# Performance work log

Hardware: AMD Instinct MI355X
Metric: run time of the kernel (lower is better)

The kernel has to match this reference:

```python
import jax, jax.numpy as jnp
import numpy as np

EPS = 1e-8
LAM = 1.0


def setup_inputs() -> dict:
    key = jax.random.key(0)
    k1, k2 = jax.random.split(key)
    B, H, W = 32, 512, 512
    output = jax.random.normal(k1, (B, 1, H, W), dtype=jnp.float32)
    target = jax.random.normal(k2, (B, 1, H, W), dtype=jnp.float32)
    return {"output": output, "target": target}


def _frc_loss(output, target):
    # squeeze channel dim: (B,1,H,W) -> (B,H,W)
    output = output[:, 0]
    target = target[:, 0]
    B, H, W = output.shape
    rnyquist = H // 2

    # radial index map (H,W): round(sqrt(fx^2 + fy^2)) in pixel-frequency units
    fx = jnp.fft.fftfreq(H, 1.0 / H)
    fy = jnp.fft.fftfreq(W, 1.0 / W)
    X, Y = jnp.meshgrid(fx, fy, indexing='ij')
    radial = jnp.round(jnp.sqrt(X ** 2 + Y ** 2)).astype(jnp.int32)
    # bins > rnyquist were ignored by the original loop -> dump into extra bin
    idx = jnp.where(radial > rnyquist, rnyquist + 1, radial).reshape(-1)  # (H*W,)

    F1 = jnp.fft.fft2(output, norm='forward')  # (B,H,W) complex
    F2 = jnp.fft.fft2(target, norm='forward')

    # per-pixel correlation terms, laid out (HW, B) for segment_sum over leading axis
    a = (F1.real * F2.real + F1.imag * F2.imag).reshape(B, -1).T
    b = (F1.imag * F2.real - F1.real * F2.imag).reshape(B, -1).T
    c1 = (F1.real ** 2 + F1.imag ** 2).reshape(B, -1).T
    c2 = (F2.real ** 2 + F2.imag ** 2).reshape(B, -1).T
    stacked = jnp.stack([a, b, c1, c2], axis=-1)  # (HW, B, 4)

    # single-pass radial-bin segment sum (replaces O(R*H*W) masked loop)
    sums = jax.ops.segment_sum(stacked, idx, num_segments=rnyquist + 2)
    sums = sums[:rnyquist + 1]  # drop overflow bin -> (rnyquist+1, B, 4)
    C_r, C_i, C1, C2 = sums[..., 0], sums[..., 1], sums[..., 2], sums[..., 3]

    frc = jnp.sqrt(C_r ** 2 + C_i ** 2) / (jnp.sqrt(C1 * C2) + EPS)
    return LAM * jnp.mean((1.0 - frc) ** 2)


def reference(output, target):
    return _frc_loss(output, target)
```

## Files before the change

kernel.cpp:

```cpp
#include <hip/hip_runtime.h>
#include <math.h>

#define NIMG 32
#define NB3  771
#define NSLICE (NIMG * 8)
#define PI_F 3.14159265358979323846f

__device__ __forceinline__ float2 cadd(float2 a, float2 b){ return make_float2(a.x+b.x, a.y+b.y); }
__device__ __forceinline__ float2 csub(float2 a, float2 b){ return make_float2(a.x-b.x, a.y-b.y); }
__device__ __forceinline__ float2 cmul(float2 a, float2 b){ return make_float2(a.x*b.x - a.y*b.y, a.x*b.y + a.y*b.x); }
__device__ __forceinline__ float2 cmul_mi(float2 a){ return make_float2(a.y, -a.x); }
__device__ __forceinline__ float2 tw(const float2* T, int m){ return T[m + (m >> 3)]; }
__device__ __forceinline__ int   sw(int pos){ return pos + (pos >> 3); }

__device__ __forceinline__ void dft8(float2* x) {
    const float c = 0.70710678118654752f;
    float2 u0 = cadd(x[0], x[4]), u1 = cadd(x[1], x[5]);
    float2 u2 = cadd(x[2], x[6]), u3 = cadd(x[3], x[7]);
    float2 v0 = csub(x[0], x[4]);
    float2 d1 = csub(x[1], x[5]);
    float2 v1 = make_float2(c*(d1.x + d1.y), c*(d1.y - d1.x));
    float2 d2 = csub(x[2], x[6]);
    float2 v2 = make_float2(d2.y, -d2.x);
    float2 d3 = csub(x[3], x[7]);
    float2 v3 = make_float2(-c*(d3.x - d3.y), -c*(d3.x + d3.y));
    float2 e0 = cadd(u0,u2), e1 = cadd(u1,u3);
    float2 f0 = csub(u0,u2), f1 = cmul_mi(csub(u1,u3));
    float2 g0 = cadd(v0,v2), g1 = cadd(v1,v3);
    float2 h0 = csub(v0,v2), h1 = cmul_mi(csub(v1,v3));
    x[0] = cadd(e0,e1); x[4] = csub(e0,e1);
    x[2] = cadd(f0,f1); x[6] = csub(f0,f1);
    x[1] = cadd(g0,g1); x[5] = csub(g0,g1);
    x[3] = cadd(h0,h1); x[7] = csub(h0,h1);
}

__device__ __forceinline__ void wave_fft512_dual(float2* Xa, float2* Xb,
                                                 float2* Sw, const float2* T,
                                                 int J) {
    dft8(Xa);
    dft8(Xb);
#pragma unroll
    for (int k = 1; k < 8; ++k) Xa[k] = cmul(Xa[k], tw(T, J * k));
#pragma unroll
    for (int k = 1; k < 8; ++k) Xb[k] = cmul(Xb[k], tw(T, J * k));
    const int jj = J + (J >> 3);
    const int j2 = J & 7;
    const int bb = 72 * (J >> 3) + j2;

#pragma unroll
    for (int k = 0; k < 8; ++k) Sw[jj + 72*k] = Xa[k];
#pragma unroll
    for (int q = 0; q < 8; ++q) Xa[q] = Sw[bb + 9*q];
#pragma unroll
    for (int k = 0; k < 8; ++k) Sw[jj + 72*k] = Xb[k];
#pragma unroll
    for (int q = 0; q < 8; ++q) Xb[q] = Sw[bb + 9*q];

    dft8(Xa);
    dft8(Xb);
#pragma unroll
    for (int k = 1; k < 8; ++k) Xa[k] = cmul(Xa[k], tw(T, 8 * j2 * k));
#pragma unroll
    for (int k = 1; k < 8; ++k) Xb[k] = cmul(Xb[k], tw(T, 8 * j2 * k));

#pragma unroll
    for (int k = 0; k < 8; ++k) Sw[bb + 9*k] = Xa[k];
#pragma unroll
    for (int q = 0; q < 8; ++q) Xa[q] = Sw[9*J + q];
#pragma unroll
    for (int k = 0; k < 8; ++k) Sw[bb + 9*k] = Xb[k];
#pragma unroll
    for (int q = 0; q < 8; ++q) Xb[q] = Sw[9*J + q];

    dft8(Xa);
    dft8(Xb);
}

__global__ __launch_bounds__(512) void fft_rows_T(const float* __restrict__ xr,
                                                  const float* __restrict__ yr,
                                                  float2* __restrict__ Zt,
                                                  float* __restrict__ sums,
                                                  unsigned int* __restrict__ counter) {
    __shared__ float2 S[8 * 576];
    __shared__ float2 T[576];
    const int t = threadIdx.x, w = t >> 6, J = t & 63;
    const int im = blockIdx.x >> 5, grp = blockIdx.x & 31;

    if (blockIdx.x < NSLICE) {
        float* z = sums + (size_t)blockIdx.x * NB3;
        for (int i = t; i < NB3; i += 512) z[i] = 0.0f;
        if (blockIdx.x == 0 && t == 0) *counter = 0u;
    }

    {
        float s, c;
        __sincosf(-2.0f * PI_F * (float)t / 512.0f, &s, &c);
        T[t + (t >> 3)] = make_float2(c, s);
    }

    const size_t b0 = ((size_t)(im * 512 + grp * 16 + w)) << 9;
    const size_t b1 = b0 + ((size_t)8 << 9);
    float2 X0[8], X1[8];
#pragma unroll
    for (int q = 0; q < 8; ++q) {
        X0[q] = make_float2(xr[b0 + J + 64*q], yr[b0 + J + 64*q]);
        X1[q] = make_float2(xr[b1 + J + 64*q], yr[b1 + J + 64*q]);
    }
    __syncthreads();

    float2* Sw = S + w * 576;
    wave_fft512_dual(X0, X1, Sw, T, J);

    const int r = ((J & 7) << 3) | (J >> 3);

#pragma unroll
    for (int k = 0; k < 8; ++k) Sw[64*k + r] = X0[k];
    __syncthreads();
    float2 eA[8];
#pragma unroll
    for (int j = 0; j < 8; ++j) eA[j] = S[j*576 + t];
    __syncthreads();

#pragma unroll
    for (int k = 0; k < 8; ++k) Sw[64*k + r] = X1[k];
    __syncthreads();
    float2 eB[8];
#pragma unroll
    for (int j = 0; j < 8; ++j) eB[j] = S[j*576 + t];

    float4* o = (float4*)(Zt + ((size_t)im << 18) + ((size_t)t << 9)
                             + (size_t)(grp * 16));
    o[0] = make_float4(eA[0].x, eA[0].y, eA[1].x, eA[1].y);
    o[1] = make_float4(eA[2].x, eA[2].y, eA[3].x, eA[3].y);
    o[2] = make_float4(eA[4].x, eA[4].y, eA[5].x, eA[5].y);
    o[3] = make_float4(eA[6].x, eA[6].y, eA[7].x, eA[7].y);
    o[4] = make_float4(eB[0].x, eB[0].y, eB[1].x, eB[1].y);
    o[5] = make_float4(eB[2].x, eB[2].y, eB[3].x, eB[3].y);
    o[6] = make_float4(eB[4].x, eB[4].y, eB[5].x, eB[5].y);
    o[7] = make_float4(eB[6].x, eB[6].y, eB[7].x, eB[7].y);
}

__global__ __launch_bounds__(256) void fft_cols_rings(const float2* __restrict__ Zt,
                                                      float* __restrict__ sums,
                                                      unsigned int* __restrict__ counter,
                                                      float* __restrict__ out) {
    __shared__ float2 S[4 * 576];
    __shared__ float2 T[576];
    __shared__ float  bins[258 * 3];
    __shared__ int    lastFlag;
    const int t = threadIdx.x, w = t >> 6, J = t & 63;
    const int im = blockIdx.x >> 6, g = blockIdx.x & 63;
    const int p = 4 * g + w;

#pragma unroll
    for (int i = 0; i < 2; ++i) {
        const int m = t + 256 * i;
        float s, c;
        __sincosf(-2.0f * PI_F * (float)m / 512.0f, &s, &c);
        T[m + (m >> 3)] = make_float2(c, s);
    }
    for (int i = t; i < 258 * 3; i += 256) bins[i] = 0.0f;

    const int c0 = (p == 0) ? 0   : p;
    const int c1 = (p == 0) ? 256 : 512 - p;
    const float2* rp0 = Zt + ((size_t)im << 18) + ((size_t)c0 << 9);
    const float2* rp1 = Zt + ((size_t)im << 18) + ((size_t)c1 << 9);
    float2 X0[8], X1[8];
#pragma unroll
    for (int q = 0; q < 8; ++q) { X0[q] = rp0[J + 64*q]; X1[q] = rp1[J + 64*q]; }
    __syncthreads();

    float2* A = S + w * 576;
    const int r  = ((J & 7) << 3) | (J >> 3);
    const int pk = r + (r >> 3);

    const float scale = 1.0f / (512.0f * 512.0f);
    auto pix = [&](float2 zk, float2 zm, float& av, float& c1v, float& c2v) {
        float f1r = 0.5f * (zk.x + zm.x) * scale;
        float f1i = 0.5f * (zk.y - zm.y) * scale;
        float f2r = 0.5f * (zk.y + zm.y) * scale;
        float f2i = 0.5f * (zm.x - zk.x) * scale;
        av  = f1r * f2r + f1i * f2i;
        c1v = f1r * f1r + f1i * f1i;
        c2v = f2r * f2r + f2i * f2i;
    };
    auto flush = [&](int ring, float a, float b, float c) {
        if (ring >= 0 && ring <= 256) {
            unsafeAtomicAdd(&bins[ring*3+0], a);
            unsafeAtomicAdd(&bins[ring*3+1], b);
            unsafeAtomicAdd(&bins[ring*3+2], c);
        }
    };

    wave_fft512_dual(X0, X1, A, T, J);

#pragma unroll
    for (int k = 0; k < 8; ++k) A[72*k + pk] = X0[k];

    float2 asv[8];
    if (p == 0) {
        int cur0 = -1;
        float a0 = 0, b0 = 0, c0v = 0;
#pragma unroll
        for (int i = 0; i < 8; ++i) {
            const int ky  = 8*J + i;
            const int kyp = (512 - ky) & 511;
            float2 zk = A[sw(ky)], zm = A[sw(kyp)];
            const float fk = (ky < 256) ? (float)ky : (float)(ky - 512);
            float av, cv, dv;
            pix(zk, zm, av, cv, dv);
            int rr = (int)rintf(fabsf(fk)); if (rr > 256) rr = 257;
            if (rr != cur0) { flush(cur0, a0, b0, c0v); cur0 = rr; a0 = av; b0 = cv; c0v = dv; }
            else            { a0 += av; b0 += cv; c0v += dv; }
        }
        flush(cur0, a0, b0, c0v);
    } else {
#pragma unroll
        for (int i = 0; i < 8; ++i) asv[i] = A[9*J + i];
    }

#pragma unroll
    for (int k = 0; k < 8; ++k) A[72*k + pk] = X1[k];

    if (p == 0) {
        int cur1 = -1;
        float a1 = 0, b1 = 0, c1v = 0;
#pragma unroll
        for (int i = 0; i < 8; ++i) {
            const int ky  = 8*J + i;
            const int kyp = (512 - ky) & 511;
            float2 zk = A[sw(ky)], zm = A[sw(kyp)];
            const float fk = (ky < 256) ? (float)ky : (float)(ky - 512);
            float av, cv, dv;
            pix(zk, zm, av, cv, dv);
            int rr = (int)rintf(sqrtf(fk*fk + 65536.0f)); if (rr > 256) rr = 257;
            if (rr != cur1) { flush(cur1, a1, b1, c1v); cur1 = rr; a1 = av; b1 = cv; c1v = dv; }
            else            { a1 += av; b1 += cv; c1v += dv; }
        }
        flush(cur1, a1, b1, c1v);
    } else {
        const float fy2 = (float)p * (float)p;
        int curR = -1;
        float sA = 0, sB = 0, sC = 0;
#pragma unroll
        for (int i = 0; i < 8; ++i) {
            const int ky  = 8*J + i;
            const int kyp = (512 - ky) & 511;
            float2 zk = asv[i];
            float2 zm = A[sw(kyp)];
            float a1v, b1v, d1v;
            pix(zk, zm, a1v, b1v, d1v);
            const float fk = (ky < 256) ? (float)ky : (float)(ky - 512);
            int rr = (int)rintf(sqrtf(fk*fk + fy2)); if (rr > 256) rr = 257;
            const float aa = 2.0f*a1v, bb = 2.0f*b1v, cc = 2.0f*d1v;
            if (rr != curR) { flush(curR, sA, sB, sC); curR = rr; sA = aa; sB = bb; sC = cc; }
            else            { sA += aa; sB += bb; sC += cc; }
        }
        flush(curR, sA, sB, sC);
    }
    __syncthreads();

    {
        float* dst = sums + (size_t)(im * 8 + (g & 7)) * NB3;
        for (int i = t; i < NB3; i += 256) unsafeAtomicAdd(&dst[i], bins[i]);
    }

    __syncthreads();
    if (t == 0) {
        __threadfence();
        unsigned int old = atomicAdd(counter, 1u);
        lastFlag = (old == (unsigned int)(gridDim.x - 1)) ? 1 : 0;
    }
    __syncthreads();
    if (lastFlag) {
        __threadfence();
        float acc = 0.0f;
        for (int idx = t; idx < NIMG * 257; idx += 256) {
            const int imQ = idx / 257;
            const int rr  = idx - imQ * 257;
            const float* pp = sums + (size_t)imQ * 8 * NB3 + rr * 3;
            float cr = 0.f, c1s = 0.f, c2s = 0.f;
#pragma unroll
            for (int s = 0; s < 8; ++s) {
                cr  += pp[(size_t)s * NB3 + 0];
                c1s += pp[(size_t)s * NB3 + 1];
                c2s += pp[(size_t)s * NB3 + 2];
            }
            float frc = fabsf(cr) / (sqrtf(c1s * c2s) + 1e-8f);
            float d = 1.0f - frc;
            acc += d * d;
        }
#pragma unroll
        for (int off = 32; off > 0; off >>= 1) acc += __shfl_down(acc, off);
        __shared__ float red[4];
        if ((t & 63) == 0) red[t >> 6] = acc;
        __syncthreads();
        if (t == 0)
            out[0] = (red[0] + red[1] + red[2] + red[3]) *
                     (1.0f / (257.0f * (float)NIMG));
    }
}

extern "C" void kernel_launch(void* const* d_in, const int* in_sizes, int n_in,
                              void* d_out, int out_size, void* d_ws, size_t ws_size,
                              hipStream_t stream) {
    const float* xr = (const float*)d_in[0];
    const float* yr = (const float*)d_in[1];

    float2* Zt = (float2*)d_ws;
    const size_t ztBytes = ((size_t)NIMG << 18) * sizeof(float2);
    float* sums = (float*)((char*)d_ws + ztBytes);
    unsigned int* counter = (unsigned int*)((char*)d_ws + ztBytes +
                              (size_t)NSLICE * NB3 * sizeof(float));

    fft_rows_T    <<<dim3(NIMG * 32), dim3(512), 0, stream>>>(xr, yr, Zt, sums, counter);
    fft_cols_rings<<<dim3(NIMG * 64), dim3(256), 0, stream>>>(Zt, sums, counter, (float*)d_out);
}
```

Before: 196.3 us.

## Use per-image completion counters and atomic-free partial bin stores

Replaces the single global last-block reduction with per-image counters, so the last of the 64 blocks for each image reduces that image's bins and atomically adds its share to the output. When the workspace is large enough, each block writes its bins to its own slot with plain stores instead of atomically adding into 8 shared slices, which also removes the zeroing pass. This spreads the tail reduction over 32 blocks instead of one serial block and removes float atomic contention. The cost is that the final loss is accumulated with float atomics, so summation order is nondeterministic.

```diff
diff --git a/kernel.cpp b/kernel.cpp
--- a/kernel.cpp
+++ b/kernel.cpp
@@ -5,6 +5,8 @@
 #define NB3  771
 #define NSLICE (NIMG * 8)
 #define PI_F 3.14159265358979323846f
+
+__device__ unsigned int g_imgCnt[NIMG];
 
 __device__ __forceinline__ float2 cadd(float2 a, float2 b){ return make_float2(a.x+b.x, a.y+b.y); }
 __device__ __forceinline__ float2 csub(float2 a, float2 b){ return make_float2(a.x-b.x, a.y-b.y); }
@@ -80,16 +82,20 @@
                                                   const float* __restrict__ yr,
                                                   float2* __restrict__ Zt,
                                                   float* __restrict__ sums,
-                                                  unsigned int* __restrict__ counter) {
+                                                  float* __restrict__ out,
+                                                  int big) {
     __shared__ float2 S[8 * 576];
     __shared__ float2 T[576];
     const int t = threadIdx.x, w = t >> 6, J = t & 63;
     const int im = blockIdx.x >> 5, grp = blockIdx.x & 31;
 
-    if (blockIdx.x < NSLICE) {
+    if (!big && blockIdx.x < NSLICE) {
         float* z = sums + (size_t)blockIdx.x * NB3;
         for (int i = t; i < NB3; i += 512) z[i] = 0.0f;
-        if (blockIdx.x == 0 && t == 0) *counter = 0u;
+    }
+    if (blockIdx.x == 0) {
+        if (t < NIMG) g_imgCnt[t] = 0u;
+        if (t == 0)   out[0] = 0.0f;
     }
 
     {
@@ -142,12 +148,12 @@
 
 __global__ __launch_bounds__(256) void fft_cols_rings(const float2* __restrict__ Zt,
                                                       float* __restrict__ sums,
-                                                      unsigned int* __restrict__ counter,
-                                                      float* __restrict__ out) {
+                                                      float* __restrict__ out,
+                                                      int big) {
     __shared__ float2 S[4 * 576];
     __shared__ float2 T[576];
     __shared__ float  bins[258 * 3];
-    __shared__ int    lastFlag;
+    __shared__ int    imFlag;
     const int t = threadIdx.x, w = t >> 6, J = t & 63;
     const int im = blockIdx.x >> 6, g = blockIdx.x & 63;
     const int p = 4 * g + w;
@@ -260,31 +266,32 @@
     }
     __syncthreads();
 
-    {
+    const int spi = big ? 64 : 8;
+    if (big) {
+        float* dst = sums + (size_t)blockIdx.x * NB3;
+        for (int i = t; i < NB3; i += 256) dst[i] = bins[i];
+    } else {
         float* dst = sums + (size_t)(im * 8 + (g & 7)) * NB3;
         for (int i = t; i < NB3; i += 256) unsafeAtomicAdd(&dst[i], bins[i]);
     }
 
+    __threadfence();
     __syncthreads();
     if (t == 0) {
+        unsigned int old = atomicAdd(&g_imgCnt[im], 1u);
+        imFlag = (old == 63u) ? 1 : 0;
+    }
+    __syncthreads();
+    if (imFlag) {
         __threadfence();
-        unsigned int old = atomicAdd(counter, 1u);
-        lastFlag = (old == (unsigned int)(gridDim.x - 1)) ? 1 : 0;
-    }
-    __syncthreads();
-    if (lastFlag) {
-        __threadfence();
+        const float* base = sums + (size_t)im * spi * NB3;
         float acc = 0.0f;
-        for (int idx = t; idx < NIMG * 257; idx += 256) {
-            const int imQ = idx / 257;
-            const int rr  = idx - imQ * 257;
-            const float* pp = sums + (size_t)imQ * 8 * NB3 + rr * 3;
+        for (int rr = t; rr < 257; rr += 256) {
             float cr = 0.f, c1s = 0.f, c2s = 0.f;
-#pragma unroll
-            for (int s = 0; s < 8; ++s) {
-                cr  += pp[(size_t)s * NB3 + 0];
-                c1s += pp[(size_t)s * NB3 + 1];
-                c2s += pp[(size_t)s * NB3 + 2];
+#pragma unroll 16
+            for (int s = 0; s < spi; ++s) {
+                const float* pp = base + (size_t)s * NB3 + rr * 3;
+                cr  += pp[0]; c1s += pp[1]; c2s += pp[2];
             }
             float frc = fabsf(cr) / (sqrtf(c1s * c2s) + 1e-8f);
             float d = 1.0f - frc;
@@ -296,8 +303,8 @@
         if ((t & 63) == 0) red[t >> 6] = acc;
         __syncthreads();
         if (t == 0)
-            out[0] = (red[0] + red[1] + red[2] + red[3]) *
-                     (1.0f / (257.0f * (float)NIMG));
+            unsafeAtomicAdd(out, (red[0] + red[1] + red[2] + red[3]) *
+                                 (1.0f / (257.0f * (float)NIMG)));
     }
 }
 
@@ -310,9 +317,8 @@
     float2* Zt = (float2*)d_ws;
     const size_t ztBytes = ((size_t)NIMG << 18) * sizeof(float2);
     float* sums = (float*)((char*)d_ws + ztBytes);
-    unsigned int* counter = (unsigned int*)((char*)d_ws + ztBytes +
-                              (size_t)NSLICE * NB3 * sizeof(float));
-
-    fft_rows_T    <<<dim3(NIMG * 32), dim3(512), 0, stream>>>(xr, yr, Zt, sums, counter);
-    fft_cols_rings<<<dim3(NIMG * 64), dim3(256), 0, stream>>>(Zt, sums, counter, (float*)d_out);
-}
+    const int big = (ws_size >= ztBytes + (size_t)2048 * NB3 * sizeof(float)) ? 1 : 0;
+
+    fft_rows_T    <<<dim3(NIMG * 32), dim3(512), 0, stream>>>(xr, yr, Zt, sums, (float*)d_out, big);
+    fft_cols_rings<<<dim3(NIMG * 64), dim3(256), 0, stream>>>(Zt, sums, (float*)d_out, big);
+}
```

Result: slower. 337.0 us (+71.7%).
